# Optimization experiments

Hardware: AMD Instinct MI355X
Metric: run time of the kernel (lower is better)

## Reference

```python
import jax, jax.numpy as jnp
import numpy as np

B, S, H = 1, 2048, 2048
NH = 16            # num attention heads
QLR = 1536         # q_lora_rank
KVLR = 512         # kv_lora_rank
DR = 64            # qk_rope_head_dim
DN = 128           # qk_nope_head_dim
DV = 128           # v_head_dim
DQK = DN + DR      # qk_head_dim = 192
EPS = 1e-6


def rmsnorm(x, w):
    xf = x.astype(jnp.float32)
    var = jnp.mean(xf * xf, axis=-1, keepdims=True)
    return (xf * jax.lax.rsqrt(var + EPS)).astype(x.dtype) * w


def rotate_half(x):
    d = x.shape[-1] // 2
    return jnp.concatenate([-x[..., d:], x[..., :d]], axis=-1)


def rope_interleave(x, cos, sin):
    # x: [b, h, s, d]; de-interleave pairs (even dims -> first half, odd -> second)
    b, h, s, d = x.shape
    x = x.reshape(b, h, s, d // 2, 2).swapaxes(-1, -2).reshape(b, h, s, d)
    return x * cos + rotate_half(x) * sin


def setup_inputs() -> dict:
    key = jax.random.key(0)
    ks = jax.random.split(key, 8)
    std = 0.02
    hidden_states = jax.random.normal(ks[0], (B, S, H), jnp.float32)
    # real rotary cos/sin for a 64-dim rope slice
    pos = jnp.arange(S, dtype=jnp.float32)
    inv_freq = 1.0 / (10000.0 ** (jnp.arange(0, DR, 2, dtype=jnp.float32) / DR))
    ang = pos[:, None] * inv_freq[None, :]            # [S, DR//2]
    emb = jnp.concatenate([ang, ang], axis=-1)        # [S, DR]
    cos = jnp.broadcast_to(jnp.cos(emb)[None], (B, S, DR)).astype(jnp.float32)
    sin = jnp.broadcast_to(jnp.sin(emb)[None], (B, S, DR)).astype(jnp.float32)
    # weights stored [in, out]
    wq_a = jax.random.normal(ks[1], (H, QLR), jnp.float32) * std
    q_ln = jnp.ones((QLR,), jnp.float32)
    wq_b = jax.random.normal(ks[2], (QLR, NH * DQK), jnp.float32) * std
    wkv_a = jax.random.normal(ks[3], (H, KVLR + DR), jnp.float32) * std
    kv_ln = jnp.ones((KVLR,), jnp.float32)
    wkv_b = jax.random.normal(ks[4], (KVLR, NH * (DN + DV)), jnp.float32) * std
    wo = jax.random.normal(ks[5], (NH * DV, H), jnp.float32) * std
    return {"hidden_states": hidden_states, "cos": cos, "sin": sin,
            "wq_a": wq_a, "q_ln": q_ln, "wq_b": wq_b,
            "wkv_a": wkv_a, "kv_ln": kv_ln, "wkv_b": wkv_b, "wo": wo}


def reference(hidden_states, cos, sin, wq_a, q_ln, wq_b, wkv_a, kv_ln, wkv_b, wo):
    b, s, _ = hidden_states.shape
    # low-rank Q: a-proj -> RMSNorm -> b-proj
    q = rmsnorm(hidden_states @ wq_a, q_ln) @ wq_b           # [b, s, NH*DQK]
    q = q.reshape(b, s, NH, DQK).transpose(0, 2, 1, 3)       # [b, NH, s, DQK]
    q_pass, q_rot = q[..., :DN], q[..., DN:]
    # compressed KV with shared rope key
    ckv = hidden_states @ wkv_a                               # [b, s, KVLR+DR]
    kv_c, k_rot = ckv[..., :KVLR], ckv[..., KVLR:]
    kv = (rmsnorm(kv_c, kv_ln) @ wkv_b).reshape(b, s, NH, DN + DV).transpose(0, 2, 1, 3)
    k_pass, v = kv[..., :DN], kv[..., DN:]
    k_rot = k_rot[:, None, :, :]                              # [b, 1, s, DR]
    cos4, sin4 = cos[:, None], sin[:, None]
    q_rot = rope_interleave(q_rot, cos4, sin4)
    k_rot = rope_interleave(k_rot, cos4, sin4)
    k_rot = jnp.broadcast_to(k_rot, (b, NH, s, DR))
    qs = jnp.concatenate([q_pass, q_rot], axis=-1)            # [b, NH, s, DQK]
    ks_ = jnp.concatenate([k_pass, k_rot], axis=-1)
    scaling = DQK ** -0.5
    scores = jnp.einsum('bhqd,bhkd->bhqk', qs, ks_) * scaling
    causal = jnp.tril(jnp.ones((s, s), bool))
    scores = jnp.where(causal, scores, jnp.finfo(scores.dtype).min)
    probs = jax.nn.softmax(scores.astype(jnp.float32), axis=-1).astype(qs.dtype)
    out = jnp.einsum('bhqk,bhkd->bhqd', probs, v)             # [b, NH, s, DV]
    out = out.transpose(0, 2, 1, 3).reshape(b, s, NH * DV)
    return out @ wo
```

## Files before the change

kernel.cpp:

```cpp
#include <hip/hip_runtime.h>
#include <hip/hip_bf16.h>
#include <stdint.h>

#define S_    2048
#define H_    2048
#define NH_   16
#define QLR_  1536
#define KVLR_ 512
#define DR_   64
#define DN_   128
#define DV_   128
#define DQK_  192
#define QW_   (NH_*DQK_)
#define KVW_  (NH_*(DN_+DV_))
#define CKVW_ (KVLR_+DR_)

typedef __attribute__((ext_vector_type(8))) short short8;
typedef __attribute__((ext_vector_type(4))) float floatx4;

__device__ __forceinline__ unsigned short f2bf(float f) {
    unsigned u = __float_as_uint(f);
    unsigned r = u + 0x7fffu + ((u >> 16) & 1u);
    return (unsigned short)(r >> 16);
}
__device__ __forceinline__ float bf2f(unsigned short h) {
    return __uint_as_float(((unsigned)h) << 16);
}
__device__ __forceinline__ void store_out(float* p, float v) { *p = v; }
__device__ __forceinline__ void store_out(unsigned short* p, float v) { *p = f2bf(v); }

typedef const __attribute__((address_space(1))) unsigned int* gas_ptr;
typedef __attribute__((address_space(3))) unsigned int* las_ptr;
__device__ __forceinline__ void gload16(const void* g, void* l) {
    __builtin_amdgcn_global_load_lds((gas_ptr)g, (las_ptr)l, 16, 0, 0);
}

__device__ __forceinline__ int xcd_swz(int orig, int nwg) {
    int q8 = nwg >> 3, r8 = nwg & 7;
    int xcd = orig & 7, jj = orig >> 3;
    return (xcd < r8 ? xcd * (q8 + 1) : r8 * (q8 + 1) + (xcd - r8) * q8) + jj;
}

#define GEMM_STAGE(b, k0) do {                                               \
        _Pragma("unroll")                                                    \
        for (int sub = 0; sub < 2; ++sub) {                                  \
            int m = tid >> 2, k8 = tid & 3;                                  \
            gload16(A + (size_t)(bm + m) * lda + (k0) + sub * 32 + k8 * 8,   \
                    &As[b][sub][tid * 8]);                                   \
        }                                                                    \
        _Pragma("unroll")                                                    \
        for (int sub = 0; sub < 2; ++sub)                                    \
            _Pragma("unroll")                                                \
            for (int j = 0; j < BN / 64; ++j) {                              \
                int ch = j * 256 + tid;                                      \
                int n = ch >> 2, k8 = ch & 3;                                \
                int nrow = bn + n; if (nrow >= N) nrow = N - 1;              \
                gload16(Bt + (size_t)nrow * K + (k0) + sub * 32 + k8 * 8,    \
                        &Bs[b][sub][ch * 8]);                                \
            }                                                                \
    } while (0)

#define GEMM_COMPUTE_SUB(sub) do {                                           \
        short8 a[2], b[NFR];                                                 \
        _Pragma("unroll")                                                    \
        for (int mi = 0; mi < 2; ++mi)                                       \
            a[mi] = *(const short8*)&As[cur][sub][(wm + mi * 16 + cc) * 32 + g * 8]; \
        _Pragma("unroll")                                                    \
        for (int ni = 0; ni < NFR; ++ni)                                     \
            b[ni] = *(const short8*)&Bs[cur][sub][(wn + ni * 16 + cc) * 32 + g * 8]; \
        __builtin_amdgcn_s_setprio(1);                                       \
        _Pragma("unroll")                                                    \
        for (int mi = 0; mi < 2; ++mi)                                       \
            _Pragma("unroll")                                                \
            for (int ni = 0; ni < NFR; ++ni)                                 \
                acc[mi][ni] = __builtin_amdgcn_mfma_f32_16x16x32_bf16(       \
                    a[mi], b[ni], acc[mi][ni], 0, 0, 0);                     \
        __builtin_amdgcn_s_setprio(0);                                       \
    } while (0)

template <typename OutT, int BN>
__global__ __launch_bounds__(256) void gemm_bf16_db(
    const unsigned short* __restrict__ A, const unsigned short* __restrict__ Bt,
    OutT* __restrict__ C, int M, int N, int K, int lda, int ldc)
{
    constexpr int NFR = BN / 32;
    __shared__ unsigned short As[2][2][64 * 32];
    __shared__ unsigned short Bs[2][2][BN * 32];

    const int tid = threadIdx.x;
    const int l = tid & 63;
    const int g = l >> 4, cc = l & 15;
    const int w = tid >> 6;
    const int wm = (w >> 1) * 32, wn = (w & 1) * (BN / 2);

    const int nwg = gridDim.x * gridDim.y;
    const int wg = xcd_swz(blockIdx.y * gridDim.x + blockIdx.x, nwg);
    const int bm = (wg / gridDim.x) * 64;
    const int bn = (wg % gridDim.x) * BN;

    floatx4 acc[2][NFR];
#pragma unroll
    for (int i = 0; i < 2; i++)
#pragma unroll
        for (int j = 0; j < NFR; j++) acc[i][j] = (floatx4){0.f, 0.f, 0.f, 0.f};

    GEMM_STAGE(0, 0);
    __syncthreads();
    int cur = 0;

    for (int k0 = 0; k0 < K; k0 += 64) {
        if (k0 + 64 < K) GEMM_STAGE(cur ^ 1, k0 + 64);
        GEMM_COMPUTE_SUB(0);
        GEMM_COMPUTE_SUB(1);
        __syncthreads();
        cur ^= 1;
    }

#pragma unroll
    for (int mi = 0; mi < 2; ++mi)
#pragma unroll
        for (int ni = 0; ni < NFR; ++ni)
#pragma unroll
            for (int i = 0; i < 4; ++i) {
                int row = bm + wm + mi * 16 + g * 4 + i;
                int col = bn + wn + ni * 16 + cc;
                if (col < N) store_out(&C[(size_t)row * ldc + col], acc[mi][ni][i]);
            }
}

__global__ __launch_bounds__(256) void gemm_bf16_dual(
    const unsigned short* __restrict__ A, const unsigned short* __restrict__ Bt,
    float* __restrict__ C0, float* __restrict__ C1,
    int M, int N, int K, int lda, int ldc0, int ldc1)
{
    constexpr int BN = 128;
    constexpr int NFR = 4;
    __shared__ unsigned short As[2][2][64 * 32];
    __shared__ unsigned short Bs[2][2][BN * 32];

    const int tid = threadIdx.x;
    const int l = tid & 63;
    const int g = l >> 4, cc = l & 15;
    const int w = tid >> 6;
    const int wm = (w >> 1) * 32, wn = (w & 1) * (BN / 2);

    const int nwg = gridDim.x * gridDim.y;
    const int wg = xcd_swz(blockIdx.y * gridDim.x + blockIdx.x, nwg);
    const int bm = (wg / gridDim.x) * 64;
    const int bn = (wg % gridDim.x) * BN;

    floatx4 acc[2][NFR];
#pragma unroll
    for (int i = 0; i < 2; i++)
#pragma unroll
        for (int j = 0; j < NFR; j++) acc[i][j] = (floatx4){0.f, 0.f, 0.f, 0.f};

    GEMM_STAGE(0, 0);
    __syncthreads();
    int cur = 0;

    for (int k0 = 0; k0 < K; k0 += 64) {
        if (k0 + 64 < K) GEMM_STAGE(cur ^ 1, k0 + 64);
        GEMM_COMPUTE_SUB(0);
        GEMM_COMPUTE_SUB(1);
        __syncthreads();
        cur ^= 1;
    }

#pragma unroll
    for (int mi = 0; mi < 2; ++mi)
#pragma unroll
        for (int ni = 0; ni < NFR; ++ni)
#pragma unroll
            for (int i = 0; i < 4; ++i) {
                int row = bm + wm + mi * 16 + g * 4 + i;
                int col = bn + wn + ni * 16 + cc;
                if (col < QLR_)
                    C0[(size_t)row * ldc0 + col] = acc[mi][ni][i];
                else if (col < N)
                    C1[(size_t)row * ldc1 + (col - QLR_)] = acc[mi][ni][i];
            }
}

__global__ __launch_bounds__(256) void gemm_bf16_pair(
    const unsigned short* __restrict__ A0, const unsigned short* __restrict__ Bt0,
    unsigned short* __restrict__ Cp0, int N0, int K0, int lda0, int ldc0, int gx0, int nwg0,
    const unsigned short* __restrict__ A1, const unsigned short* __restrict__ Bt1,
    unsigned short* __restrict__ Cp1, int N1, int K1, int lda1, int ldc1, int gx1, int nwg1)
{
    constexpr int BN = 128;
    constexpr int NFR = 4;
    __shared__ unsigned short As[2][2][64 * 32];
    __shared__ unsigned short Bs[2][2][BN * 32];

    const int tid = threadIdx.x;
    const int l = tid & 63;
    const int g = l >> 4, cc = l & 15;
    const int w = tid >> 6;
    const int wm = (w >> 1) * 32, wn = (w & 1) * (BN / 2);

    const int bid = blockIdx.x;
    const unsigned short *A, *Bt;
    unsigned short* C;
    int N, K, lda, ldc, wg, gx;
    if (bid < nwg0) {
        wg = xcd_swz(bid, nwg0); gx = gx0;
        A = A0; Bt = Bt0; C = Cp0; N = N0; K = K0; lda = lda0; ldc = ldc0;
    } else {
        wg = xcd_swz(bid - nwg0, nwg1); gx = gx1;
        A = A1; Bt = Bt1; C = Cp1; N = N1; K = K1; lda = lda1; ldc = ldc1;
    }
    const int bm = (wg / gx) * 64;
    const int bn = (wg % gx) * BN;

    floatx4 acc[2][NFR];
#pragma unroll
    for (int i = 0; i < 2; i++)
#pragma unroll
        for (int j = 0; j < NFR; j++) acc[i][j] = (floatx4){0.f, 0.f, 0.f, 0.f};

    GEMM_STAGE(0, 0);
    __syncthreads();
    int cur = 0;

    for (int k0 = 0; k0 < K; k0 += 64) {
        if (k0 + 64 < K) GEMM_STAGE(cur ^ 1, k0 + 64);
        GEMM_COMPUTE_SUB(0);
        GEMM_COMPUTE_SUB(1);
        __syncthreads();
        cur ^= 1;
    }

#pragma unroll
    for (int mi = 0; mi < 2; ++mi)
#pragma unroll
        for (int ni = 0; ni < NFR; ++ni)
#pragma unroll
            for (int i = 0; i < 4; ++i) {
                int row = bm + wm + mi * 16 + g * 4 + i;
                int col = bn + wn + ni * 16 + cc;
                if (col < N) C[(size_t)row * ldc + col] = f2bf(acc[mi][ni][i]);
            }
}

__global__ __launch_bounds__(256) void cast_bf16(
    const float* __restrict__ in, unsigned short* __restrict__ out, int n)
{
    int i = (blockIdx.x * 256 + threadIdx.x) * 4;
    if (i >= n) return;
    float4 v = *(const float4*)&in[i];
    ushort4 u;
    u.x = f2bf(v.x); u.y = f2bf(v.y); u.z = f2bf(v.z); u.w = f2bf(v.w);
    *(ushort4*)&out[i] = u;
}

__global__ __launch_bounds__(256) void transpose_cast(
    const float* __restrict__ W, unsigned short* __restrict__ Wt, int K, int N,
    float scl)
{
    __shared__ float t[32][33];
    const int n0 = blockIdx.x * 32, k0 = blockIdx.y * 32;
    const int tx = threadIdx.x & 31, ty4 = (threadIdx.x >> 5) * 4;
#pragma unroll
    for (int j = 0; j < 4; ++j)
        t[ty4 + j][tx] = W[(size_t)(k0 + ty4 + j) * N + n0 + tx];
    __syncthreads();
#pragma unroll
    for (int j = 0; j < 4; ++j)
        Wt[(size_t)(n0 + ty4 + j) * K + k0 + tx] = f2bf(t[tx][ty4 + j] * scl);
}

__global__ __launch_bounds__(256) void rmsnorm_bf16out(
    const float* __restrict__ x, const float* __restrict__ w,
    unsigned short* __restrict__ y, int cols, int xstride)
{
    const float* xr = x + (size_t)blockIdx.x * xstride;
    unsigned short* yr = y + (size_t)blockIdx.x * cols;
    const int tid = threadIdx.x;
    float ss = 0.f;
    for (int c = tid; c < cols; c += 256) { float v = xr[c]; ss += v * v; }
#pragma unroll
    for (int off = 32; off > 0; off >>= 1) ss += __shfl_xor(ss, off);
    __shared__ float red[4];
    if ((tid & 63) == 0) red[tid >> 6] = ss;
    __syncthreads();
    ss = red[0] + red[1] + red[2] + red[3];
    const float inv = rsqrtf(ss / (float)cols + 1e-6f);
    for (int c = tid; c < cols; c += 256) yr[c] = f2bf(xr[c] * inv * w[c]);
}

__global__ void rope_q_bf(unsigned short* __restrict__ q,
                          const float* __restrict__ cs, const float* __restrict__ sn)
{
    int t = blockIdx.x * 256 + threadIdx.x;
    int chunk = t >> 5, j = t & 31;
    int s = chunk >> 4, h = chunk & 15;
    unsigned short* x = q + (size_t)s * QW_ + h * DQK_ + DN_;
    float e = bf2f(x[2 * j]), o = bf2f(x[2 * j + 1]);
    float c = cs[s * DR_ + j], si = sn[s * DR_ + j];
    unsigned short u = f2bf(e * c - o * si);
    unsigned short v = f2bf(o * c + e * si);
    x[j] = u; x[j + 32] = v;
}

__global__ __launch_bounds__(256) void prep_k(
    const unsigned short* __restrict__ kvb, const float* __restrict__ ckv,
    const float* __restrict__ cs, const float* __restrict__ sn,
    unsigned short* __restrict__ kg)
{
    const int s = blockIdx.x, tid = threadIdx.x;
    __shared__ unsigned short rot[64];
    if (tid < 32) {
        int j = tid;
        const float* x = ckv + (size_t)s * CKVW_ + KVLR_;
        float e = x[2 * j], o = x[2 * j + 1];
        float c = cs[s * DR_ + j], si = sn[s * DR_ + j];
        rot[j] = f2bf(e * c - o * si);
        rot[j + 32] = f2bf(o * c + e * si);
    }
    __syncthreads();
    const int sw = s & 7;
    for (int ch = tid; ch < 384; ch += 256) {
        int hh = ch / 24, d8 = ch % 24;
        short8 v;
        if (d8 < 16)
            v = *(const short8*)&kvb[(size_t)s * KVW_ + hh * 256 + d8 * 8];
        else
            v = *(const short8*)&rot[(d8 - 16) * 8];
        int d8s = d8 ^ sw;
        *(short8*)&kg[((size_t)hh * S_ + s) * 192 + d8s * 8] = v;
    }
}

__global__ __launch_bounds__(256) void transpose_v(
    const unsigned short* __restrict__ kvb, unsigned short* __restrict__ vt)
{
    __shared__ unsigned short t[32][36];
    const int dv0 = blockIdx.x * 32, s0 = blockIdx.y * 32, h = blockIdx.z;
    const int r = threadIdx.x >> 3, c4 = threadIdx.x & 7;
    ushort4 ld = *(const ushort4*)&kvb[(size_t)(s0 + r) * KVW_ + h * 256 + 128 + dv0 + c4 * 4];
    t[r][c4 * 4 + 0] = ld.x; t[r][c4 * 4 + 1] = ld.y;
    t[r][c4 * 4 + 2] = ld.z; t[r][c4 * 4 + 3] = ld.w;
    __syncthreads();
    ushort4 st;
    st.x = t[c4 * 4 + 0][r]; st.y = t[c4 * 4 + 1][r];
    st.z = t[c4 * 4 + 2][r]; st.w = t[c4 * 4 + 3][r];
    *(ushort4*)&vt[(size_t)(h * 128 + dv0 + r) * S_ + s0 + c4 * 4] = st;
}

__global__ __launch_bounds__(256, 3) void flash_attn7(
    const unsigned short* __restrict__ qg, const unsigned short* __restrict__ kg,
    const unsigned short* __restrict__ vt,
    unsigned short* __restrict__ op0, unsigned short* __restrict__ op1,
    float* __restrict__ mlp)
{
    const int bid = blockIdx.x;
    const int qblk = 31 - (bid >> 5);
    const int low5 = bid & 31;
    const int h = low5 & 15;
    const int sp = low5 >> 4;
    const int pb = h * 32 + qblk;

    __shared__ unsigned short sm[2 * 6144 + 2 * 4096 + 4 * 640];
    unsigned short* Kb = sm;
    unsigned short* Vb = sm + 12288;
    const int tid = threadIdx.x;
    const int w = tid >> 6;
    const int l = tid & 63, g = l >> 4, cc = l & 15;
    unsigned short* Pw = sm + 20480 + w * 640;

    const int qmin = qblk * 64 + w * 16;
    const int q_lane = qmin + cc;
    const int wave_qmax = qmin + 15;
    const int HT = qblk + 1;
    const int kt_begin = sp * HT, kt_end = kt_begin + HT;

    const unsigned short* kh = kg + (size_t)h * S_ * 192;
    const unsigned short* vh = vt + (size_t)(h * 128) * S_;

    short8 qf[6];
    {
        const unsigned short* qb = qg + (size_t)q_lane * QW_ + h * DQK_;
#pragma unroll
        for (int k6 = 0; k6 < 6; ++k6)
            qf[k6] = *(const short8*)&qb[k6 * 32 + g * 8];
    }

    floatx4 accO[8];
#pragma unroll
    for (int nt = 0; nt < 8; ++nt) accO[nt] = (floatx4){0.f, 0.f, 0.f, 0.f};
    float m_r = -1e30f, l_r = 0.f;

#define STAGE_KV(b, kt) do {                                             \
        const unsigned short* ksrc = kh + (size_t)(kt) * 32 * 192;       \
        _Pragma("unroll")                                                \
        for (int j = 0; j < 3; ++j) {                                    \
            int ch = j * 256 + tid;                                      \
            gload16(ksrc + ch * 8, Kb + (b) * 6144 + ch * 8);            \
        }                                                                \
        const int krow = (kt) * 32;                                      \
        _Pragma("unroll")                                                \
        for (int j = 0; j < 2; ++j) {                                    \
            int ch = j * 256 + tid;                                      \
            int dv = ch >> 2, j8 = ch & 3;                               \
            gload16(vh + (size_t)dv * S_ + krow + j8 * 8,                \
                    Vb + (b) * 4096 + ch * 8);                           \
        }                                                                \
    } while (0)

    STAGE_KV(0, kt_begin);
    int cur = 0;

    for (int kt = kt_begin; kt < kt_end; ++kt) {
        const int krow0 = kt * 32;
        __syncthreads();
        if (kt + 1 < kt_end) STAGE_KV(cur ^ 1, kt + 1);

        if (krow0 <= wave_qmax) {
            const unsigned short* Kc = Kb + cur * 6144;
            const unsigned short* Vc = Vb + cur * 4096;
            const int swz = (cc & 7) << 3;

            floatx4 s0 = (floatx4){0.f, 0.f, 0.f, 0.f};
            floatx4 s1 = (floatx4){0.f, 0.f, 0.f, 0.f};
            __builtin_amdgcn_s_setprio(1);
#pragma unroll
            for (int k6 = 0; k6 < 6; ++k6) {
                short8 b0 = *(const short8*)&Kc[cc * 192 + ((k6 * 32 + g * 8) ^ swz)];
                short8 b1 = *(const short8*)&Kc[(16 + cc) * 192 + ((k6 * 32 + g * 8) ^ swz)];
                s0 = __builtin_amdgcn_mfma_f32_16x16x32_bf16(b0, qf[k6], s0, 0, 0, 0);
                s1 = __builtin_amdgcn_mfma_f32_16x16x32_bf16(b1, qf[k6], s1, 0, 0, 0);
            }
            __builtin_amdgcn_s_setprio(0);

            float v0[4], v1[4];
            if (krow0 + 31 <= qmin) {
#pragma unroll
                for (int i = 0; i < 4; ++i) { v0[i] = s0[i]; v1[i] = s1[i]; }
            } else {
#pragma unroll
                for (int i = 0; i < 4; ++i) {
                    v0[i] = (krow0 + g * 4 + i) <= q_lane ? s0[i] : -1e30f;
                    v1[i] = (krow0 + 16 + g * 4 + i) <= q_lane ? s1[i] : -1e30f;
                }
            }
            float mt = fmaxf(fmaxf(fmaxf(v0[0], v0[1]), fmaxf(v0[2], v0[3])),
                             fmaxf(fmaxf(v1[0], v1[1]), fmaxf(v1[2], v1[3])));
            mt = fmaxf(mt, __shfl_xor(mt, 16));
            mt = fmaxf(mt, __shfl_xor(mt, 32));

            if (!__all(mt <= m_r + 6.0f)) {
                float mn = fmaxf(m_r, mt);
                float alpha = exp2f(m_r - mn);
                m_r = mn;
                l_r *= alpha;
                float aB[4];
#pragma unroll
                for (int i = 0; i < 4; ++i) aB[i] = __shfl(alpha, g * 4 + i);
#pragma unroll
                for (int nt = 0; nt < 8; ++nt)
#pragma unroll
                    for (int i = 0; i < 4; ++i) accO[nt][i] *= aB[i];
            }

            float p0[4], p1[4], ps = 0.f;
#pragma unroll
            for (int i = 0; i < 4; ++i) {
                p0[i] = exp2f(v0[i] - m_r);
                p1[i] = exp2f(v1[i] - m_r);
                ps += p0[i] + p1[i];
            }
            ps += __shfl_xor(ps, 16);
            ps += __shfl_xor(ps, 32);
            l_r += ps;

            {
                unsigned pk00, pk01, pk10, pk11;
                asm("v_cvt_pk_bf16_f32 %0, %1, %2" : "=v"(pk00) : "v"(p0[0]), "v"(p0[1]));
                asm("v_cvt_pk_bf16_f32 %0, %1, %2" : "=v"(pk01) : "v"(p0[2]), "v"(p0[3]));
                asm("v_cvt_pk_bf16_f32 %0, %1, %2" : "=v"(pk10) : "v"(p1[0]), "v"(p1[1]));
                asm("v_cvt_pk_bf16_f32 %0, %1, %2" : "=v"(pk11) : "v"(p1[2]), "v"(p1[3]));
                uint2 w0, w1;
                w0.x = pk00; w0.y = pk01;
                w1.x = pk10; w1.y = pk11;
                *(uint2*)&Pw[cc * 40 + g * 4] = w0;
                *(uint2*)&Pw[cc * 40 + 16 + g * 4] = w1;
            }

            short8 pf = *(const short8*)&Pw[cc * 40 + g * 8];
            __builtin_amdgcn_s_setprio(1);
#pragma unroll
            for (int nt = 0; nt < 8; ++nt) {
                short8 vr = *(const short8*)&Vc[(nt * 16 + cc) * 32 + g * 8];
                accO[nt] = __builtin_amdgcn_mfma_f32_16x16x32_bf16(pf, vr, accO[nt], 0, 0, 0);
            }
            __builtin_amdgcn_s_setprio(0);
        }
        cur ^= 1;
    }
#undef STAGE_KV

    float mB[4], lB[4];
#pragma unroll
    for (int i = 0; i < 4; ++i) {
        int src = (g << 4) | (g * 4 + i);
        mB[i] = __shfl(m_r, src);
        lB[i] = __shfl(l_r, src);
    }
    unsigned short* op = sp ? op1 : op0;
#pragma unroll
    for (int nt = 0; nt < 8; ++nt)
#pragma unroll
        for (int i = 0; i < 4; ++i)
            op[(size_t)pb * 8192 + (w * 16 + g * 4 + i) * 128 + nt * 16 + cc] =
                f2bf(accO[nt][i]);
    if (cc == 0) {
#pragma unroll
        for (int i = 0; i < 4; ++i) {
            size_t mi = ((size_t)(sp * 512 + pb) * 64 + w * 16 + g * 4 + i) * 2;
            mlp[mi + 0] = mB[i];
            mlp[mi + 1] = lB[i];
        }
    }
}

__global__ __launch_bounds__(256) void merge_attn(
    const unsigned short* __restrict__ op0, const unsigned short* __restrict__ op1,
    const float* __restrict__ mlp, unsigned short* __restrict__ ao)
{
    const int pb = blockIdx.x;
    const int h = pb >> 5, qblk = pb & 31;
    const int tid = threadIdx.x;
    const int row = tid >> 2, c0 = (tid & 3) * 32;

    const size_t mi0 = ((size_t)pb * 64 + row) * 2;
    const size_t mi1 = ((size_t)(512 + pb) * 64 + row) * 2;
    float m0 = mlp[mi0 + 0], l0 = mlp[mi0 + 1];
    float m1 = mlp[mi1 + 0], l1 = mlp[mi1 + 1];
    float mf = fmaxf(m0, m1);
    float e0 = exp2f(m0 - mf), e1 = exp2f(m1 - mf);
    float inv = 1.f / (l0 * e0 + l1 * e1);
    float w0 = e0 * inv, w1 = e1 * inv;

    const size_t pbase = (size_t)pb * 8192 + row * 128 + c0;
    unsigned short* dst = ao + (size_t)(qblk * 64 + row) * (NH_ * DV_) + h * DV_ + c0;
#pragma unroll
    for (int j = 0; j < 4; ++j) {
        short8 a = *(const short8*)&op0[pbase + j * 8];
        short8 b = *(const short8*)&op1[pbase + j * 8];
        short8 o;
#pragma unroll
        for (int k = 0; k < 8; ++k)
            o[k] = (short)f2bf(bf2f((unsigned short)a[k]) * w0 +
                               bf2f((unsigned short)b[k]) * w1);
        *(short8*)&dst[j * 8] = o;
    }
}

extern "C" void kernel_launch(void* const* d_in, const int* in_sizes, int n_in,
                              void* d_out, int out_size, void* d_ws, size_t ws_size,
                              hipStream_t stream)
{
    const float* hs    = (const float*)d_in[0];
    const float* cosp  = (const float*)d_in[1];
    const float* sinp  = (const float*)d_in[2];
    const float* wq_a  = (const float*)d_in[3];
    const float* q_ln  = (const float*)d_in[4];
    const float* wq_b  = (const float*)d_in[5];
    const float* wkv_a = (const float*)d_in[6];
    const float* kv_ln = (const float*)d_in[7];
    const float* wkv_b = (const float*)d_in[8];
    const float* wo    = (const float*)d_in[9];
    float* out = (float*)d_out;

    char* ws = (char*)d_ws;
    float*          qa     = (float*)(ws);
    float*          ckv    = (float*)(ws + 12582912);
    unsigned short* q_bf   = (unsigned short*)(ws + 17301504);
    unsigned short* kvb    = (unsigned short*)(ws + 29884416);
    unsigned short* hs_bf  = (unsigned short*)(ws + 46661632);
    unsigned short* qa_bf  = (unsigned short*)(ws + 55050240);
    unsigned short* ckv_bf = (unsigned short*)(ws + 61341696);
    unsigned short* ao_bf  = (unsigned short*)(ws + 63438848);
    unsigned short* wt     = (unsigned short*)(ws + 71827456);
    unsigned short* kg     = (unsigned short*)qa;
    unsigned short* vtb    = hs_bf;
    unsigned short* wbt2   = (unsigned short*)qa;

    unsigned short* op0 = qa_bf;
    unsigned short* op1 = wt;
    float*          mlp = ckv;

    const float qscale = 0.07216878364870322f * 1.4426950408889634f;

    cast_bf16<<<(S_ * H_) / 1024, 256, 0, stream>>>(hs, hs_bf, S_ * H_);

    transpose_cast<<<dim3(QLR_ / 32, H_ / 32), 256, 0, stream>>>(wq_a, wt, H_, QLR_, 1.f);
    transpose_cast<<<dim3(CKVW_ / 32, H_ / 32), 256, 0, stream>>>(
        wkv_a, wt + (size_t)QLR_ * H_, H_, CKVW_, 1.f);
    gemm_bf16_dual<<<dim3((QLR_ + CKVW_ + 127) / 128, S_ / 64), 256, 0, stream>>>(
        hs_bf, wt, qa, ckv, S_, QLR_ + CKVW_, H_, H_, QLR_, CKVW_);
    rmsnorm_bf16out<<<S_, 256, 0, stream>>>(qa, q_ln, qa_bf, QLR_, QLR_);
    rmsnorm_bf16out<<<S_, 256, 0, stream>>>(ckv, kv_ln, ckv_bf, KVLR_, CKVW_);

    transpose_cast<<<dim3(QW_ / 32, QLR_ / 32), 256, 0, stream>>>(wq_b, wt, QLR_, QW_, qscale);
    transpose_cast<<<dim3(KVW_ / 32, KVLR_ / 32), 256, 0, stream>>>(wkv_b, wbt2, KVLR_, KVW_, 1.f);
    gemm_bf16_pair<<<768 + 1024, 256, 0, stream>>>(
        qa_bf, wt, q_bf, QW_, QLR_, QLR_, QW_, QW_ / 128, 768,
        ckv_bf, wbt2, kvb, KVW_, KVLR_, KVLR_, KVW_, KVW_ / 128, 1024);
    rope_q_bf<<<(S_ * NH_ * 32) / 256, 256, 0, stream>>>(q_bf, cosp, sinp);

    prep_k<<<S_, 256, 0, stream>>>(kvb, ckv, cosp, sinp, kg);
    transpose_v<<<dim3(4, 64, 16), 256, 0, stream>>>(kvb, vtb);

    flash_attn7<<<1024, 256, 0, stream>>>(q_bf, kg, vtb, op0, op1, mlp);
    merge_attn<<<512, 256, 0, stream>>>(op0, op1, mlp, ao_bf);

    transpose_cast<<<dim3(H_ / 32, H_ / 32), 256, 0, stream>>>(wo, wt, H_, H_, 1.f);
    gemm_bf16_db<float, 128><<<dim3(H_ / 128, S_ / 64), 256, 0, stream>>>(
        ao_bf, wt, out, S_, H_, NH_ * DV_, NH_ * DV_, H_);
}
```

Before: 214.2 us.

## Enlarge pair GEMM tiles to 128x128 with 32-wide K steps

The paired Q-b/KV-b projection GEMM moves from 64x128 tiles to 128x128 tiles, with each wave computing a 64x64 sub-tile (4x4 MFMA fragments). It also steps K by 32 instead of 64 using a new staging macro, and raises wave priority around the MFMA burst. The aim is more arithmetic per byte loaded and fewer workgroups (896 instead of 1792). In exchange each thread holds more accumulator registers, the grid is smaller, and barriers come twice as often per unit of K.

```diff
diff --git a/kernel.cpp b/kernel.cpp
--- a/kernel.cpp
+++ b/kernel.cpp
@@ -182,22 +182,38 @@
             }
 }
 
+#define PAIR_STAGE(b, k0) do {                                               \
+        _Pragma("unroll")                                                    \
+        for (int j = 0; j < 2; ++j) {                                        \
+            int ch = j * 256 + tid;                                          \
+            int m = ch >> 2, k8 = ch & 3;                                    \
+            gload16(A + (size_t)(bm + m) * lda + (k0) + k8 * 8,              \
+                    &As[b][ch * 8]);                                         \
+        }                                                                    \
+        _Pragma("unroll")                                                    \
+        for (int j = 0; j < 2; ++j) {                                        \
+            int ch = j * 256 + tid;                                          \
+            int n = ch >> 2, k8 = ch & 3;                                    \
+            int nrow = bn + n; if (nrow >= N) nrow = N - 1;                  \
+            gload16(Bt + (size_t)nrow * K + (k0) + k8 * 8,                   \
+                    &Bs[b][ch * 8]);                                         \
+        }                                                                    \
+    } while (0)
+
 __global__ __launch_bounds__(256) void gemm_bf16_pair(
     const unsigned short* __restrict__ A0, const unsigned short* __restrict__ Bt0,
     unsigned short* __restrict__ Cp0, int N0, int K0, int lda0, int ldc0, int gx0, int nwg0,
     const unsigned short* __restrict__ A1, const unsigned short* __restrict__ Bt1,
     unsigned short* __restrict__ Cp1, int N1, int K1, int lda1, int ldc1, int gx1, int nwg1)
 {
-    constexpr int BN = 128;
-    constexpr int NFR = 4;
-    __shared__ unsigned short As[2][2][64 * 32];
-    __shared__ unsigned short Bs[2][2][BN * 32];
+    __shared__ unsigned short As[2][128 * 32];
+    __shared__ unsigned short Bs[2][128 * 32];
 
     const int tid = threadIdx.x;
     const int l = tid & 63;
     const int g = l >> 4, cc = l & 15;
     const int w = tid >> 6;
-    const int wm = (w >> 1) * 32, wn = (w & 1) * (BN / 2);
+    const int wm = (w >> 1) * 64, wn = (w & 1) * 64;
 
     const int bid = blockIdx.x;
     const unsigned short *A, *Bt;
@@ -210,31 +226,45 @@
         wg = xcd_swz(bid - nwg0, nwg1); gx = gx1;
         A = A1; Bt = Bt1; C = Cp1; N = N1; K = K1; lda = lda1; ldc = ldc1;
     }
-    const int bm = (wg / gx) * 64;
-    const int bn = (wg % gx) * BN;
-
-    floatx4 acc[2][NFR];
-#pragma unroll
-    for (int i = 0; i < 2; i++)
-#pragma unroll
-        for (int j = 0; j < NFR; j++) acc[i][j] = (floatx4){0.f, 0.f, 0.f, 0.f};
-
-    GEMM_STAGE(0, 0);
+    const int bm = (wg / gx) * 128;
+    const int bn = (wg % gx) * 128;
+
+    floatx4 acc[4][4];
+#pragma unroll
+    for (int i = 0; i < 4; i++)
+#pragma unroll
+        for (int j = 0; j < 4; j++) acc[i][j] = (floatx4){0.f, 0.f, 0.f, 0.f};
+
+    PAIR_STAGE(0, 0);
     __syncthreads();
     int cur = 0;
 
-    for (int k0 = 0; k0 < K; k0 += 64) {
-        if (k0 + 64 < K) GEMM_STAGE(cur ^ 1, k0 + 64);
-        GEMM_COMPUTE_SUB(0);
-        GEMM_COMPUTE_SUB(1);
+    for (int k0 = 0; k0 < K; k0 += 32) {
+        if (k0 + 32 < K) PAIR_STAGE(cur ^ 1, k0 + 32);
+
+        short8 a[4], b[4];
+#pragma unroll
+        for (int mi = 0; mi < 4; ++mi)
+            a[mi] = *(const short8*)&As[cur][(wm + mi * 16 + cc) * 32 + g * 8];
+#pragma unroll
+        for (int ni = 0; ni < 4; ++ni)
+            b[ni] = *(const short8*)&Bs[cur][(wn + ni * 16 + cc) * 32 + g * 8];
+        __builtin_amdgcn_s_setprio(1);
+#pragma unroll
+        for (int mi = 0; mi < 4; ++mi)
+#pragma unroll
+            for (int ni = 0; ni < 4; ++ni)
+                acc[mi][ni] = __builtin_amdgcn_mfma_f32_16x16x32_bf16(
+                    a[mi], b[ni], acc[mi][ni], 0, 0, 0);
+        __builtin_amdgcn_s_setprio(0);
         __syncthreads();
         cur ^= 1;
     }
 
 #pragma unroll
-    for (int mi = 0; mi < 2; ++mi)
-#pragma unroll
-        for (int ni = 0; ni < NFR; ++ni)
+    for (int mi = 0; mi < 4; ++mi)
+#pragma unroll
+        for (int ni = 0; ni < 4; ++ni)
 #pragma unroll
             for (int i = 0; i < 4; ++i) {
                 int row = bm + wm + mi * 16 + g * 4 + i;
@@ -605,9 +635,9 @@
 
     transpose_cast<<<dim3(QW_ / 32, QLR_ / 32), 256, 0, stream>>>(wq_b, wt, QLR_, QW_, qscale);
     transpose_cast<<<dim3(KVW_ / 32, KVLR_ / 32), 256, 0, stream>>>(wkv_b, wbt2, KVLR_, KVW_, 1.f);
-    gemm_bf16_pair<<<768 + 1024, 256, 0, stream>>>(
-        qa_bf, wt, q_bf, QW_, QLR_, QLR_, QW_, QW_ / 128, 768,
-        ckv_bf, wbt2, kvb, KVW_, KVLR_, KVLR_, KVW_, KVW_ / 128, 1024);
+    gemm_bf16_pair<<<384 + 512, 256, 0, stream>>>(
+        qa_bf, wt, q_bf, QW_, QLR_, QLR_, QW_, QW_ / 128, 384,
+        ckv_bf, wbt2, kvb, KVW_, KVLR_, KVLR_, KVW_, KVW_ / 128, 512);
     rope_q_bf<<<(S_ * NH_ * 32) / 256, 256, 0, stream>>>(q_bf, cosp, sinp);
 
     prep_k<<<S_, 256, 0, stream>>>(kvb, ckv, cosp, sinp, kg);
```

Measured after the change: 211.9 us, median of 2. About the same (-1.1%).
